# Kernel tuning notes

Hardware: AMD Instinct MI355X
Metric: run time of the kernel (lower is better)

The kernel has to match this reference:

```python
import jax, jax.numpy as jnp
import numpy as np

D_MODEL = 2048
D_INNER = 4096   # expand * d_model == ngroups * d_state
D_XB = 1024
N_HEADS = 32     # = ngroups
HEAD_DIM = 128   # = d_state
N_KV_HEADS = D_XB // HEAD_DIM  # 8
N_REP = N_HEADS // N_KV_HEADS  # 4
D_IN_PROJ = D_INNER + 2 * D_XB + D_INNER + N_HEADS  # 10272
ROPE_BASE = 10000.0


def setup_inputs() -> dict:
    key = jax.random.key(0)
    k1, k2, k3 = jax.random.split(key, 3)
    u = jax.random.normal(k1, (2, 2048, D_MODEL), dtype=jnp.float32)
    W_in = jax.random.normal(k2, (D_IN_PROJ, D_MODEL), dtype=jnp.float32) * (1.0 / np.sqrt(D_MODEL))
    W_out = jax.random.normal(k3, (D_MODEL, D_INNER), dtype=jnp.float32) * (1.0 / np.sqrt(D_INNER))
    return {"u": u, "W_in": W_in, "W_out": W_out}


def _rotate_half(x):
    x1, x2 = jnp.split(x, 2, axis=-1)
    return jnp.concatenate((-x2, x1), axis=-1)


def _rope_cos_sin(seqlen, dim, dtype):
    inv_freq = 1.0 / (ROPE_BASE ** (jnp.arange(0, dim, 2, dtype=jnp.float32) / dim))
    pos = jnp.arange(seqlen, dtype=jnp.float32)
    freqs = pos[:, None] * inv_freq[None, :]          # [S, dim/2]
    emb = jnp.concatenate((freqs, freqs), axis=-1)    # [S, dim]
    return jnp.cos(emb).astype(dtype), jnp.sin(emb).astype(dtype)


def reference(u, W_in, W_out):
    # NOTE: the module's forward short-circuits (early return) into a GQA
    # attention path; the SSM code after the return is dead.
    B, S, _ = u.shape
    zxbcdt = jnp.einsum('bsd,ed->bse', u, W_in)       # [B, S, D_IN_PROJ]
    # split: z (d_inner), x (d_xb), B (d_xb), C (d_inner), dt (nheads); d_mlp = 0
    o0 = D_INNER
    x = zxbcdt[..., o0:o0 + D_XB]
    Bm = zxbcdt[..., o0 + D_XB:o0 + 2 * D_XB]
    C = zxbcdt[..., o0 + 2 * D_XB:o0 + 2 * D_XB + D_INNER]
    # q = C (32 heads), k = B (8 heads), v = x (8 heads); [B, H, S, Dh]
    q = C.reshape(B, S, N_HEADS, HEAD_DIM).transpose(0, 2, 1, 3)
    k = Bm.reshape(B, S, N_KV_HEADS, HEAD_DIM).transpose(0, 2, 1, 3)
    v = x.reshape(B, S, N_KV_HEADS, HEAD_DIM).transpose(0, 2, 1, 3)
    cos, sin = _rope_cos_sin(S, HEAD_DIM, u.dtype)    # [S, Dh]
    cos = cos[None, None]                             # [1, 1, S, Dh]
    sin = sin[None, None]
    q = q * cos + _rotate_half(q) * sin
    k = k * cos + _rotate_half(k) * sin
    # repeat_kv: repeat_interleave along head dim
    k = jnp.repeat(k, N_REP, axis=1)
    v = jnp.repeat(v, N_REP, axis=1)
    scale = 1.0 / np.sqrt(HEAD_DIM)
    scores = jnp.einsum('bhqd,bhkd->bhqk', q, k) * scale
    causal = jnp.tril(jnp.ones((S, S), dtype=bool))
    scores = jnp.where(causal[None, None], scores, jnp.finfo(scores.dtype).min)
    attn = jax.nn.softmax(scores, axis=-1)
    out = jnp.einsum('bhqk,bhkd->bhqd', attn, v)      # [B, H, S, Dh]
    out = out.transpose(0, 2, 1, 3).reshape(B, S, D_INNER)
    return jnp.einsum('bse,de->bsd', out, W_out)      # [B, S, d_model]
```

## Files before the change

kernel.cpp:

```cpp
#include <hip/hip_runtime.h>
#include <stdint.h>

#define S_LEN 2048
#define BATCH 2
#define NH 32
#define NKV 8
#define HD 128
#define NE 6144

typedef __attribute__((ext_vector_type(8))) short short8;
typedef __attribute__((ext_vector_type(4))) float floatx4;

__device__ __forceinline__ unsigned short f2bf(float f) {
    union { float f; uint32_t u; } v; v.f = f;
    uint32_t u = v.u;
    u += 0x7FFFu + ((u >> 16) & 1u);
    return (unsigned short)(u >> 16);
}
__device__ __forceinline__ float bf2f(unsigned short h) {
    union { uint32_t u; float f; } v; v.u = ((uint32_t)h) << 16;
    return v.f;
}

__global__ void cast_f32_bf16(const float* __restrict__ in,
                              unsigned short* __restrict__ out, int n4) {
    int i = blockIdx.x * blockDim.x + threadIdx.x;
    if (i >= n4) return;
    float4 f = reinterpret_cast<const float4*>(in)[i];
    ushort4 o;
    o.x = f2bf(f.x); o.y = f2bf(f.y); o.z = f2bf(f.z); o.w = f2bf(f.w);
    reinterpret_cast<ushort4*>(out)[i] = o;
}

template <int OUT_BF16>
__global__ void __launch_bounds__(256)
gemm_bt(const unsigned short* __restrict__ A, const unsigned short* __restrict__ Bt,
        void* __restrict__ Cv, int M, int N, int K) {
    __shared__ unsigned short As[128 * 32];
    __shared__ unsigned short Bs[128 * 32];
    const int tid  = threadIdx.x;
    const int w    = tid >> 6;
    const int lane = tid & 63;
    const int quad = lane >> 4;
    const int l16  = lane & 15;
    const int wm   = w >> 1, wn = w & 1;
    const int m0 = blockIdx.y * 128, n0 = blockIdx.x * 128;

    floatx4 acc[4][4];
#pragma unroll
    for (int i = 0; i < 4; i++)
#pragma unroll
        for (int j = 0; j < 4; j++) acc[i][j] = {0.f, 0.f, 0.f, 0.f};

    const int lr = lane >> 2;
    const int lk = (lane & 3) * 8;
    const int KT = K >> 5;

    for (int kt = 0; kt < KT; ++kt) {
        const int k0 = kt << 5;
        __syncthreads();
#pragma unroll
        for (int c = 0; c < 2; ++c) {
            const int chunk = w * 2 + c;
            const unsigned short* ga = A  + (size_t)(m0 + chunk * 16 + lr) * K + k0 + lk;
            __builtin_amdgcn_global_load_lds(
                (const __attribute__((address_space(1))) void*)ga,
                (__attribute__((address_space(3))) void*)(As + chunk * 512), 16, 0, 0);
            const unsigned short* gb = Bt + (size_t)(n0 + chunk * 16 + lr) * K + k0 + lk;
            __builtin_amdgcn_global_load_lds(
                (const __attribute__((address_space(1))) void*)gb,
                (__attribute__((address_space(3))) void*)(Bs + chunk * 512), 16, 0, 0);
        }
        __syncthreads();
        short8 af[4], bf[4];
#pragma unroll
        for (int t = 0; t < 4; ++t) {
            af[t] = *reinterpret_cast<const short8*>(As + (wm * 64 + t * 16 + l16) * 32 + quad * 8);
            bf[t] = *reinterpret_cast<const short8*>(Bs + (wn * 64 + t * 16 + l16) * 32 + quad * 8);
        }
#pragma unroll
        for (int i = 0; i < 4; i++)
#pragma unroll
            for (int j = 0; j < 4; j++)
                acc[i][j] = __builtin_amdgcn_mfma_f32_16x16x32_bf16(af[i], bf[j], acc[i][j], 0, 0, 0);
    }

#pragma unroll
    for (int i = 0; i < 4; i++)
#pragma unroll
        for (int j = 0; j < 4; j++) {
            const int row = m0 + wm * 64 + i * 16 + quad * 4;
            const int col = n0 + wn * 64 + j * 16 + l16;
#pragma unroll
            for (int r = 0; r < 4; r++) {
                float vv = acc[i][j][r];
                if (OUT_BF16)
                    ((unsigned short*)Cv)[(size_t)(row + r) * N + col] = f2bf(vv);
                else
                    ((float*)Cv)[(size_t)(row + r) * N + col] = vv;
            }
        }
}

#define QSCALE 0.12748539509360f
__global__ void rope_split(const unsigned short* __restrict__ Z,
                           unsigned short* __restrict__ Q,
                           unsigned short* __restrict__ Kb,
                           unsigned short* __restrict__ Vt) {
    const int PER_TOK = 2048 + 512 + 1024;
    int idx = blockIdx.x * blockDim.x + threadIdx.x;
    if (idx >= BATCH * S_LEN * PER_TOK) return;
    int t = idx / PER_TOK;
    int r = idx - t * PER_TOK;
    int b = t / S_LEN, s = t - b * S_LEN;
    const unsigned short* z = Z + (size_t)t * NE;
    if (r < 2048) {
        int h = r >> 6, j = r & 63;
        float x0 = bf2f(z[2048 + h * 128 + j]);
        float x1 = bf2f(z[2048 + h * 128 + j + 64]);
        float inv = exp2f((float)j * -0.20762050593f);
        float c, sn; sincosf((float)s * inv, &sn, &c);
        size_t base = ((size_t)(b * NH + h) * S_LEN + s) * HD;
        Q[base + j]      = f2bf((x0 * c - x1 * sn) * QSCALE);
        Q[base + j + 64] = f2bf((x1 * c + x0 * sn) * QSCALE);
    } else if (r < 2560) {
        int rr = r - 2048; int kh = rr >> 6, j = rr & 63;
        float x0 = bf2f(z[1024 + kh * 128 + j]);
        float x1 = bf2f(z[1024 + kh * 128 + j + 64]);
        float inv = exp2f((float)j * -0.20762050593f);
        float c, sn; sincosf((float)s * inv, &sn, &c);
        size_t base = ((size_t)(b * NKV + kh) * S_LEN + s) * HD;
        Kb[base + j]      = f2bf(x0 * c - x1 * sn);
        Kb[base + j + 64] = f2bf(x1 * c + x0 * sn);
    } else {
        int m = r - 2560; int kh = m >> 7, d = m & 127;
        Vt[((size_t)(b * NKV + kh) * HD + d) * S_LEN + s] = z[m];
    }
}

__global__ void __launch_bounds__(256)
attn_kernel(const unsigned short* __restrict__ Q,
            const unsigned short* __restrict__ Kb,
            const unsigned short* __restrict__ Vt,
            unsigned short* __restrict__ Ob) {
    __shared__ unsigned short Ks[64 * 128];
    __shared__ unsigned short Vs[128 * 64];
    __shared__ unsigned short Ps[4][16 * 64];
    const int tid  = threadIdx.x;
    const int w    = tid >> 6;
    const int lane = tid & 63;
    const int quad = lane >> 4;
    const int l16  = lane & 15;
    const int blk = blockIdx.x;
    const int qt = 31 - (blk >> 6);
    const int bh = blk & 63;
    const int h = bh & 31, b = bh >> 5;
    const int kvh = h >> 2;
    const int qw0 = qt * 64 + w * 16;

    const unsigned short* Qbase = Q  + ((size_t)(b * NH  + h)   * S_LEN) * HD;
    const unsigned short* Kbase = Kb + ((size_t)(b * NKV + kvh) * S_LEN) * HD;
    const unsigned short* Vbase = Vt + ((size_t)(b * NKV + kvh) * HD) * S_LEN;

    short8 qf[4];
    {
        const unsigned short* qrow = Qbase + (size_t)(qw0 + l16) * HD + quad * 8;
#pragma unroll
        for (int ks = 0; ks < 4; ++ks)
            qf[ks] = *reinterpret_cast<const short8*>(qrow + ks * 32);
    }

    floatx4 oacc[8];
#pragma unroll
    for (int i = 0; i < 8; i++) oacc[i] = {0.f, 0.f, 0.f, 0.f};
    float lsum[4] = {0.f, 0.f, 0.f, 0.f};

    const int s_row = (lane >> 4);
    const int k_pc  = lane & 15;
    const int v_pc  = lane & 7;
    const int kv_end = qt * 64 + 64;

    for (int kv0 = 0; kv0 < kv_end; kv0 += 64) {
        __syncthreads();
#pragma unroll
        for (int c = 0; c < 4; ++c) {
            const int bI = w * 4 + c;
            const int row = bI * 4 + s_row;
            const int lc = k_pc ^ (row & 7);
            const unsigned short* ga = Kbase + (size_t)(kv0 + row) * HD + lc * 8;
            __builtin_amdgcn_global_load_lds(
                (const __attribute__((address_space(1))) void*)ga,
                (__attribute__((address_space(3))) void*)(Ks + bI * 512), 16, 0, 0);
        }
#pragma unroll
        for (int c = 0; c < 4; ++c) {
            const int bI = w * 4 + c;
            const int drow = bI * 8 + (lane >> 3);
            const int lc = v_pc ^ (drow & 7);
            const unsigned short* ga = Vbase + (size_t)drow * S_LEN + kv0 + lc * 8;
            __builtin_amdgcn_global_load_lds(
                (const __attribute__((address_space(1))) void*)ga,
                (__attribute__((address_space(3))) void*)(Vs + bI * 512), 16, 0, 0);
        }
        __syncthreads();

        if (kv0 <= qw0 + 15) {
            const bool diag = (kv0 + 63 > qw0);
            floatx4 sacc[4];
#pragma unroll
            for (int nt = 0; nt < 4; nt++) sacc[nt] = {0.f, 0.f, 0.f, 0.f};
#pragma unroll
            for (int ks = 0; ks < 4; ++ks) {
#pragma unroll
                for (int nt = 0; nt < 4; ++nt) {
                    const int srow = nt * 16 + l16;
                    const int pc = (ks * 4 + quad) ^ (l16 & 7);
                    short8 kf = *reinterpret_cast<const short8*>(Ks + srow * 128 + pc * 8);
                    sacc[nt] = __builtin_amdgcn_mfma_f32_16x16x32_bf16(qf[ks], kf, sacc[nt], 0, 0, 0);
                }
            }
            unsigned short* pw = &Ps[w][0];
#pragma unroll
            for (int nt = 0; nt < 4; ++nt) {
                const int col = kv0 + nt * 16 + l16;
                const int cch = nt * 2 + (l16 >> 3);
#pragma unroll
                for (int r = 0; r < 4; ++r) {
                    const int row = qw0 + quad * 4 + r;
                    float p = (!diag || col <= row) ? exp2f(sacc[nt][r]) : 0.0f;
                    lsum[r] += p;
                    const int prow = quad * 4 + r;
                    const int pc = cch ^ (prow & 7);
                    pw[prow * 64 + pc * 8 + (l16 & 7)] = f2bf(p);
                }
            }
#pragma unroll
            for (int kv_sub = 0; kv_sub < 2; ++kv_sub) {
                const int pcP = (kv_sub * 4 + quad) ^ (l16 & 7);
                short8 pf = *reinterpret_cast<const short8*>(pw + l16 * 64 + pcP * 8);
#pragma unroll
                for (int dt = 0; dt < 8; ++dt) {
                    const int drow = dt * 16 + l16;
                    const int pcV = (kv_sub * 4 + quad) ^ (l16 & 7);
                    short8 vf = *reinterpret_cast<const short8*>(Vs + drow * 64 + pcV * 8);
                    oacc[dt] = __builtin_amdgcn_mfma_f32_16x16x32_bf16(pf, vf, oacc[dt], 0, 0, 0);
                }
            }
        }
    }

    float linv[4];
#pragma unroll
    for (int r = 0; r < 4; ++r) {
        float s = lsum[r];
#pragma unroll
        for (int off = 1; off < 16; off <<= 1) s += __shfl_xor(s, off);
        linv[r] = 1.0f / s;
    }
#pragma unroll
    for (int dt = 0; dt < 8; ++dt) {
        const int d = dt * 16 + l16;
#pragma unroll
        for (int r = 0; r < 4; ++r) {
            const int row = qw0 + quad * 4 + r;
            Ob[((size_t)(b * S_LEN + row)) * 4096 + h * 128 + d] = f2bf(oacc[dt][r] * linv[r]);
        }
    }
}

extern "C" void kernel_launch(void* const* d_in, const int* in_sizes, int n_in,
                              void* d_out, int out_size, void* d_ws, size_t ws_size,
                              hipStream_t stream) {
    const float* u     = (const float*)d_in[0];
    const float* W_in  = (const float*)d_in[1];
    const float* W_out = (const float*)d_in[2];
    float* out = (float*)d_out;

    char* ws = (char*)d_ws;
    unsigned short* u_bf    = (unsigned short*)(ws);
    unsigned short* win_bf  = (unsigned short*)(ws + 16777216);
    unsigned short* wout_bf = (unsigned short*)(ws + 41943040);
    unsigned short* Z       = (unsigned short*)(ws + 58720256);
    unsigned short* Qb      = (unsigned short*)(ws + 109051904);
    unsigned short* Kv      = (unsigned short*)(ws + 142606336);
    unsigned short* Vt      = (unsigned short*)(ws + 150994944);
    unsigned short* Ob      = (unsigned short*)(ws + 159383552);

    {
        int n4 = (2 * 2048 * 2048) / 4;
        cast_f32_bf16<<<(n4 + 255) / 256, 256, 0, stream>>>(u, u_bf, n4);
        n4 = (6144 * 2048) / 4;
        cast_f32_bf16<<<(n4 + 255) / 256, 256, 0, stream>>>(W_in + (size_t)4096 * 2048, win_bf, n4);
        n4 = (2048 * 4096) / 4;
        cast_f32_bf16<<<(n4 + 255) / 256, 256, 0, stream>>>(W_out, wout_bf, n4);
    }
    {
        dim3 g(6144 / 128, 4096 / 128);
        gemm_bt<1><<<g, 256, 0, stream>>>(u_bf, win_bf, Z, 4096, 6144, 2048);
    }
    {
        int n = BATCH * S_LEN * 3584;
        rope_split<<<(n + 255) / 256, 256, 0, stream>>>(Z, Qb, Kv, Vt);
    }
    attn_kernel<<<BATCH * NH * (S_LEN / 64), 256, 0, stream>>>(Qb, Kv, Vt, Ob);
    {
        dim3 g(2048 / 128, 4096 / 128);
        gemm_bt<0><<<g, 256, 0, stream>>>(Ob, wout_bf, out, 4096, 2048, 4096);
    }
}
```

Baseline: 560.2 us.

## Double-buffer K/V tiles in attention kernel and pad P scratch layout

The attention kernel now keeps two K/V shared-memory buffers and issues the global-to-LDS loads for the next tile before computing the current one, so memory traffic overlaps with MFMA work instead of waiting behind a barrier each iteration. The P scratch buffer switches from an XOR swizzle to a padded 72-element row stride, which simplifies its addressing. MFMA sections are wrapped in s_setprio raises. In exchange, shared-memory use roughly doubles, which may lower occupancy, and warps no longer skip fully masked work on the diagonal tile.

New measurement: 560.2 us. About the same (+0.0%).

```diff
diff --git a/kernel.cpp b/kernel.cpp
--- a/kernel.cpp
+++ b/kernel.cpp
@@ -143,9 +143,9 @@
             const unsigned short* __restrict__ Kb,
             const unsigned short* __restrict__ Vt,
             unsigned short* __restrict__ Ob) {
-    __shared__ unsigned short Ks[64 * 128];
-    __shared__ unsigned short Vs[128 * 64];
-    __shared__ unsigned short Ps[4][16 * 64];
+    __shared__ unsigned short Ks[2][64 * 128];
+    __shared__ unsigned short Vs[2][64 * 128];
+    __shared__ unsigned short Ps[4][16 * 72];
     const int tid  = threadIdx.x;
     const int w    = tid >> 6;
     const int lane = tid & 63;
@@ -175,79 +175,101 @@
     for (int i = 0; i < 8; i++) oacc[i] = {0.f, 0.f, 0.f, 0.f};
     float lsum[4] = {0.f, 0.f, 0.f, 0.f};
 
-    const int s_row = (lane >> 4);
-    const int k_pc  = lane & 15;
-    const int v_pc  = lane & 7;
-    const int kv_end = qt * 64 + 64;
-
-    for (int kv0 = 0; kv0 < kv_end; kv0 += 64) {
-        __syncthreads();
-#pragma unroll
-        for (int c = 0; c < 4; ++c) {
-            const int bI = w * 4 + c;
-            const int row = bI * 4 + s_row;
-            const int lc = k_pc ^ (row & 7);
-            const unsigned short* ga = Kbase + (size_t)(kv0 + row) * HD + lc * 8;
-            __builtin_amdgcn_global_load_lds(
-                (const __attribute__((address_space(1))) void*)ga,
-                (__attribute__((address_space(3))) void*)(Ks + bI * 512), 16, 0, 0);
-        }
-#pragma unroll
-        for (int c = 0; c < 4; ++c) {
-            const int bI = w * 4 + c;
-            const int drow = bI * 8 + (lane >> 3);
-            const int lc = v_pc ^ (drow & 7);
-            const unsigned short* ga = Vbase + (size_t)drow * S_LEN + kv0 + lc * 8;
-            __builtin_amdgcn_global_load_lds(
-                (const __attribute__((address_space(1))) void*)ga,
-                (__attribute__((address_space(3))) void*)(Vs + bI * 512), 16, 0, 0);
-        }
-        __syncthreads();
-
-        if (kv0 <= qw0 + 15) {
-            const bool diag = (kv0 + 63 > qw0);
-            floatx4 sacc[4];
-#pragma unroll
-            for (int nt = 0; nt < 4; nt++) sacc[nt] = {0.f, 0.f, 0.f, 0.f};
-#pragma unroll
-            for (int ks = 0; ks < 4; ++ks) {
-#pragma unroll
-                for (int nt = 0; nt < 4; ++nt) {
-                    const int srow = nt * 16 + l16;
-                    const int pc = (ks * 4 + quad) ^ (l16 & 7);
-                    short8 kf = *reinterpret_cast<const short8*>(Ks + srow * 128 + pc * 8);
-                    sacc[nt] = __builtin_amdgcn_mfma_f32_16x16x32_bf16(qf[ks], kf, sacc[nt], 0, 0, 0);
-                }
+    const unsigned short* kp[4];
+    const unsigned short* vp[4];
+#pragma unroll
+    for (int c = 0; c < 4; ++c) {
+        const int bI = w * 4 + c;
+        const int krow = bI * 4 + (lane >> 4);
+        kp[c] = Kbase + (size_t)krow * HD + ((lane & 15) ^ (krow & 7)) * 8;
+        const int drow = bI * 8 + (lane >> 3);
+        vp[c] = Vbase + (size_t)drow * S_LEN + ((lane & 7) ^ (drow & 7)) * 8;
+    }
+
+    const int NT = qt + 1;
+
+#define STAGE(BUF) do {                                                        \
+    unsigned short* kd = &Ks[BUF][0];                                          \
+    unsigned short* vd = &Vs[BUF][0];                                          \
+    _Pragma("unroll")                                                          \
+    for (int c = 0; c < 4; ++c) {                                              \
+        const int bI = w * 4 + c;                                              \
+        __builtin_amdgcn_global_load_lds(                                      \
+            (const __attribute__((address_space(1))) void*)kp[c],              \
+            (__attribute__((address_space(3))) void*)(kd + bI * 512), 16, 0, 0);\
+        __builtin_amdgcn_global_load_lds(                                      \
+            (const __attribute__((address_space(1))) void*)vp[c],              \
+            (__attribute__((address_space(3))) void*)(vd + bI * 512), 16, 0, 0);\
+        kp[c] += 64 * HD; vp[c] += 64;                                         \
+    }                                                                          \
+} while (0)
+
+    STAGE(0);
+    asm volatile("s_waitcnt vmcnt(0)" ::: "memory");
+    __builtin_amdgcn_s_barrier();
+    asm volatile("" ::: "memory");
+
+    unsigned short* pw  = &Ps[w][0];
+    unsigned short* pst = pw + quad * 288 + l16;
+    const unsigned short* prd = pw + l16 * 72 + quad * 8;
+
+    int cur = 0;
+    for (int t = 0; t < NT; ++t) {
+        if (t + 1 < NT) STAGE(cur ^ 1);
+
+        const bool diag = (t == qt);
+        const int kv0 = t << 6;
+        const unsigned short* Kc = &Ks[cur][0];
+        const unsigned short* Vc = &Vs[cur][0];
+
+        floatx4 sacc[4];
+#pragma unroll
+        for (int nb = 0; nb < 4; nb++) sacc[nb] = {0.f, 0.f, 0.f, 0.f};
+        __builtin_amdgcn_s_setprio(1);
+#pragma unroll
+        for (int ks = 0; ks < 4; ++ks) {
+#pragma unroll
+            for (int nb = 0; nb < 4; ++nb) {
+                const int srow = nb * 16 + l16;
+                const int pc = (ks * 4 + quad) ^ (l16 & 7);
+                short8 kf = *reinterpret_cast<const short8*>(Kc + srow * 128 + pc * 8);
+                sacc[nb] = __builtin_amdgcn_mfma_f32_16x16x32_bf16(qf[ks], kf, sacc[nb], 0, 0, 0);
             }
-            unsigned short* pw = &Ps[w][0];
-#pragma unroll
-            for (int nt = 0; nt < 4; ++nt) {
-                const int col = kv0 + nt * 16 + l16;
-                const int cch = nt * 2 + (l16 >> 3);
-#pragma unroll
-                for (int r = 0; r < 4; ++r) {
-                    const int row = qw0 + quad * 4 + r;
-                    float p = (!diag || col <= row) ? exp2f(sacc[nt][r]) : 0.0f;
-                    lsum[r] += p;
-                    const int prow = quad * 4 + r;
-                    const int pc = cch ^ (prow & 7);
-                    pw[prow * 64 + pc * 8 + (l16 & 7)] = f2bf(p);
-                }
+        }
+        __builtin_amdgcn_s_setprio(0);
+
+#pragma unroll
+        for (int nb = 0; nb < 4; ++nb) {
+            const int col = kv0 + nb * 16 + l16;
+#pragma unroll
+            for (int r = 0; r < 4; ++r) {
+                const int row = qw0 + quad * 4 + r;
+                float p = (!diag || col <= row) ? exp2f(sacc[nb][r]) : 0.0f;
+                lsum[r] += p;
+                pst[r * 72 + nb * 16] = f2bf(p);
             }
-#pragma unroll
-            for (int kv_sub = 0; kv_sub < 2; ++kv_sub) {
-                const int pcP = (kv_sub * 4 + quad) ^ (l16 & 7);
-                short8 pf = *reinterpret_cast<const short8*>(pw + l16 * 64 + pcP * 8);
-#pragma unroll
-                for (int dt = 0; dt < 8; ++dt) {
-                    const int drow = dt * 16 + l16;
-                    const int pcV = (kv_sub * 4 + quad) ^ (l16 & 7);
-                    short8 vf = *reinterpret_cast<const short8*>(Vs + drow * 64 + pcV * 8);
-                    oacc[dt] = __builtin_amdgcn_mfma_f32_16x16x32_bf16(pf, vf, oacc[dt], 0, 0, 0);
-                }
+        }
+
+        __builtin_amdgcn_s_setprio(1);
+#pragma unroll
+        for (int kv_sub = 0; kv_sub < 2; ++kv_sub) {
+            short8 pf = *reinterpret_cast<const short8*>(prd + kv_sub * 32);
+#pragma unroll
+            for (int dt = 0; dt < 8; ++dt) {
+                const int drow = dt * 16 + l16;
+                const int pcV = (kv_sub * 4 + quad) ^ (l16 & 7);
+                short8 vf = *reinterpret_cast<const short8*>(Vc + drow * 64 + pcV * 8);
+                oacc[dt] = __builtin_amdgcn_mfma_f32_16x16x32_bf16(pf, vf, oacc[dt], 0, 0, 0);
             }
         }
-    }
+        __builtin_amdgcn_s_setprio(0);
+
+        asm volatile("s_waitcnt vmcnt(0)" ::: "memory");
+        __builtin_amdgcn_s_barrier();
+        asm volatile("" ::: "memory");
+        cur ^= 1;
+    }
+#undef STAGE
 
     float linv[4];
 #pragma unroll
```
